# Kernel optimization log

Measured on AMD Instinct MI355X. Metric: run time of the kernel, lower is better.

## Reference

```python
import jax, jax.numpy as jnp
import numpy as np

WD, WH, WW = 4, 8, 8
N_WIN = WD * WH * WW  # 256 tokens per window
NUM_HEADS = 8
DIM = 512
HIDDEN = int(DIM * 4.0)
SHIFT = (2, 4, 4)
EPS = 1e-5


def _rel_pos_index():
    coords = np.stack(np.meshgrid(np.arange(WD), np.arange(WH), np.arange(WW), indexing='ij'))
    cf = coords.reshape(3, -1)  # [3, N]
    rc = cf[:, :, None] - cf[:, None, :]  # [3, N, N]
    rc = rc.transpose(1, 2, 0).astype(np.int64)
    rc[:, :, 0] += WD - 1
    rc[:, :, 1] += WH - 1
    rc[:, :, 2] += WW - 1
    rc[:, :, 0] *= (2 * WH - 1) * (2 * WW - 1)
    rc[:, :, 1] *= (2 * WW - 1)
    return jnp.asarray(rc.sum(-1))  # [N, N]

REL_IDX = _rel_pos_index()


def setup_inputs() -> dict:
    key = jax.random.key(0)
    ks = jax.random.split(key, 10)
    B, D, H, W = 1, 16, 64, 64
    L = D * H * W
    s = 0.02
    table_size = (2 * WD - 1) * (2 * WH - 1) * (2 * WW - 1)  # 1575
    return {
        'x': jax.random.normal(ks[0], (B, L, DIM), jnp.float32),
        't_emb': jax.random.normal(ks[1], (B, DIM), jnp.float32),
        'ada_w': jax.random.normal(ks[2], (DIM, 6 * DIM), jnp.float32) * s,
        'ada_b': jnp.zeros((6 * DIM,), jnp.float32),
        'rel_table': jax.random.normal(ks[3], (table_size, NUM_HEADS), jnp.float32) * s,
        'qkv_w': jax.random.normal(ks[4], (DIM, 3 * DIM), jnp.float32) * s,
        'qkv_b': jnp.zeros((3 * DIM,), jnp.float32),
        'proj_w': jax.random.normal(ks[5], (DIM, DIM), jnp.float32) * s,
        'proj_b': jnp.zeros((DIM,), jnp.float32),
        'fc1_w': jax.random.normal(ks[6], (DIM, HIDDEN), jnp.float32) * s,
        'fc1_b': jnp.zeros((HIDDEN,), jnp.float32),
        'fc2_w': jax.random.normal(ks[7], (HIDDEN, DIM), jnp.float32) * s,
        'fc2_b': jnp.zeros((DIM,), jnp.float32),
        'D': D, 'H': H, 'W': W,
    }


def _layernorm(y):
    m = jnp.mean(y, axis=-1, keepdims=True)
    v = jnp.mean(jnp.square(y - m), axis=-1, keepdims=True)
    return (y - m) * jax.lax.rsqrt(v + EPS)


def _window_partition(x3, D, H, W):
    B, _, _, _, C = x3.shape
    x3 = x3.reshape(B, D // WD, WD, H // WH, WH, W // WW, WW, C)
    x3 = x3.transpose(0, 1, 3, 5, 2, 4, 6, 7)
    return x3.reshape(-1, N_WIN, C)


def _window_reverse(win, B, D, H, W):
    C = win.shape[-1]
    x3 = win.reshape(B, D // WD, H // WH, W // WW, WD, WH, WW, C)
    x3 = x3.transpose(0, 1, 4, 2, 5, 3, 6, 7)
    return x3.reshape(B, D, H, W, C)


def _window_attention(xn, rel_table, qkv_w, qkv_b, proj_w, proj_b):
    Bn, N, C = xn.shape
    h, d = NUM_HEADS, C // NUM_HEADS
    qkv = (xn @ qkv_w + qkv_b).reshape(Bn, N, 3, h, d).transpose(2, 0, 3, 1, 4)
    q, k, v = qkv[0], qkv[1], qkv[2]
    scale = d ** -0.5
    attn = jnp.einsum('bhnd,bhmd->bhnm', q * scale, k)  # [Bn, h, N, N]
    bias = rel_table[REL_IDX]  # gather -> [N, N, h]
    attn = jax.nn.softmax(attn + bias.transpose(2, 0, 1)[None], axis=-1)
    o = jnp.einsum('bhnm,bhmd->bhnd', attn, v)
    o = o.transpose(0, 2, 1, 3).reshape(Bn, N, C)
    return o @ proj_w + proj_b


def reference(x, t_emb, ada_w, ada_b, rel_table, qkv_w, qkv_b, proj_w, proj_b,
              fc1_w, fc1_b, fc2_w, fc2_b, D, H, W):
    B, L, C = x.shape
    mod = jax.nn.silu(t_emb) @ ada_w + ada_b  # [B, 6C]
    shift_msa, scale_msa, gate_msa, shift_mlp, scale_mlp, gate_mlp = jnp.split(mod, 6, axis=-1)

    x3 = x.reshape(B, D, H, W, C)
    x3 = jnp.roll(x3, shift=(-SHIFT[0], -SHIFT[1], -SHIFT[2]), axis=(1, 2, 3))
    xw = _window_partition(x3, D, H, W)  # [B*nW, N, C]

    xn = _layernorm(xw) * (1.0 + scale_msa[:, None, :]) + shift_msa[:, None, :]
    attn_out = _window_attention(xn, rel_table, qkv_w, qkv_b, proj_w, proj_b)
    xw = xw + gate_msa[:, None, :] * attn_out

    x3 = _window_reverse(xw, B, D, H, W)
    x3 = jnp.roll(x3, shift=SHIFT, axis=(1, 2, 3))
    x = x3.reshape(B, L, C)

    xn = _layernorm(x) * (1.0 + scale_mlp[:, None, :]) + shift_mlp[:, None, :]
    h1 = jax.nn.gelu(xn @ fc1_w + fc1_b, approximate=False)
    mlp_out = h1 @ fc2_w + fc2_b
    return x + gate_mlp[:, None, :] * mlp_out
```

## Files before the change

### kernel.cpp

```cpp
#include <hip/hip_runtime.h>
#include <hip/hip_bf16.h>
#include <math.h>


typedef __attribute__((ext_vector_type(8))) short short8;
typedef __attribute__((ext_vector_type(4))) short bs4;
typedef __attribute__((ext_vector_type(4))) float f32x4;

typedef const __attribute__((address_space(1))) unsigned int gu32;
typedef __attribute__((address_space(3))) unsigned int lu32;

__device__ __forceinline__ float bf2f(short s) {
  unsigned int u = ((unsigned int)(unsigned short)s) << 16;
  float f;
  __builtin_memcpy(&f, &u, 4);
  return f;
}
__device__ __forceinline__ short f2bf(float f) {
  unsigned int u;
  __builtin_memcpy(&u, &f, 4);
  u += 0x7FFFu + ((u >> 16) & 1u);
  return (short)(u >> 16);
}
__device__ __forceinline__ short f2bf_trunc(float f) {
  unsigned int u;
  __builtin_memcpy(&u, &f, 4);
  return (short)(u >> 16);
}

__device__ __forceinline__ int win_to_src(int p) {
  int wi = p >> 8, t = p & 255;
  int sd = (((wi >> 6) << 2) + (t >> 6) + 2) & 15;
  int sh = ((((wi >> 3) & 7) << 3) + ((t >> 3) & 7) + 4) & 63;
  int sw = (((wi & 7) << 3) + (t & 7) + 4) & 63;
  return (sd << 12) | (sh << 6) | sw;
}

__global__ __launch_bounds__(256) void mod_kernel(
    const float* __restrict__ t_emb, const float* __restrict__ ada_w,
    const float* __restrict__ ada_b, float* __restrict__ mod) {
  __shared__ float sl[512];
  int tid = threadIdx.x;
  for (int r = 0; r < 2; ++r) {
    float x = t_emb[r * 256 + tid];
    sl[r * 256 + tid] = x / (1.f + expf(-x));
  }
  __syncthreads();
  int col = blockIdx.x * 256 + tid;
  float acc = ada_b[col];
  for (int k = 0; k < 512; ++k)
    acc += sl[k] * ada_w[(size_t)k * 3072 + col];
  mod[col] = acc;
}

__global__ __launch_bounds__(256) void bias_kernel(
    const float* __restrict__ rel_table, short* __restrict__ biasT) {
  int head = blockIdx.x >> 8;
  int j = blockIdx.x & 255;
  int i = threadIdx.x;
  int di = i >> 6, hi = (i >> 3) & 7, wi = i & 7;
  int dj = j >> 6, hj = (j >> 3) & 7, wj = j & 7;
  int idx = (di - dj + 3) * 225 + (hi - hj + 7) * 15 + (wi - wj + 7);
  biasT[(size_t)blockIdx.x * 256 + i] = f2bf(rel_table[idx * 8 + head]);
}

__global__ __launch_bounds__(256) void transpose_kernel(
    const float* __restrict__ in, short* __restrict__ out, int K, int N) {
  __shared__ short t[32][33];
  int n0 = blockIdx.x * 32, k0 = blockIdx.y * 32;
  int tx = threadIdx.x & 31, ty = threadIdx.x >> 5;
#pragma unroll
  for (int r = 0; r < 4; ++r)
    t[ty + r * 8][tx] = f2bf(in[(size_t)(k0 + ty + r * 8) * N + n0 + tx]);
  __syncthreads();
#pragma unroll
  for (int r = 0; r < 4; ++r)
    out[(size_t)(n0 + ty + r * 8) * K + k0 + tx] = t[tx][ty + r * 8];
}

template <int GATHER>
__global__ __launch_bounds__(256) void ln_kernel(
    const float* __restrict__ xin, short* __restrict__ xout,
    const float* __restrict__ shv, const float* __restrict__ scv) {
  int wave = threadIdx.x >> 6, lane = threadIdx.x & 63;
  int p = blockIdx.x * 4 + wave;
  int s = GATHER ? win_to_src(p) : p;
  const f32x4* px = (const f32x4*)(xin + (size_t)s * 512 + lane * 8);
  f32x4 a = px[0], b = px[1];
  float xs[8];
#pragma unroll
  for (int j = 0; j < 4; ++j) { xs[j] = a[j]; xs[4 + j] = b[j]; }
  float sum = 0.f, sq = 0.f;
#pragma unroll
  for (int j = 0; j < 8; ++j) { sum += xs[j]; sq += xs[j] * xs[j]; }
#pragma unroll
  for (int off = 1; off < 64; off <<= 1) {
    sum += __shfl_xor(sum, off, 64);
    sq += __shfl_xor(sq, off, 64);
  }
  float mean = sum * (1.f / 512.f);
  float var = sq * (1.f / 512.f) - mean * mean;
  float rs = rsqrtf(var + 1e-5f);
  short8 o;
#pragma unroll
  for (int j = 0; j < 8; ++j) {
    int c = lane * 8 + j;
    float val = (xs[j] - mean) * rs * (1.f + scv[c]) + shv[c];
    o[j] = f2bf(val);
  }
  *(short8*)(xout + (size_t)p * 512 + lane * 8) = o;
}

template <int EPI>
__global__ __launch_bounds__(256) void gemm_kernel(
    const short* __restrict__ A, const short* __restrict__ BT,
    const float* __restrict__ bias, void* __restrict__ Cv,
    int M, int N, int K, int nbn,
    const float* __restrict__ resid, const float* __restrict__ gate) {
  __shared__ __align__(16) short Atl[128 * 64];
  __shared__ __align__(16) short Btl[128 * 64];

  int nwg = gridDim.x;
  int bid = blockIdx.x;
  int q = nwg >> 3, r = nwg & 7;
  int xcd = bid & 7, idx = bid >> 3;
  int swz = (xcd < r ? xcd * (q + 1) : r * (q + 1) + (xcd - r) * q) + idx;
  int bm = swz / nbn, bn = swz % nbn;

  int tid = threadIdx.x;
  int lane = tid & 63, wave = tid >> 6;
  int l15 = lane & 15, lg = lane >> 4;
  int wr = (wave >> 1) * 64, wc = (wave & 1) * 64;

  const size_t rowb = (size_t)K * 2;
  const char* ga[4];
  const char* gb[4];
  char* la[4];
  char* lb[4];
#pragma unroll
  for (int rr = 0; rr < 4; ++rr) {
    int o = rr * 4096 + tid * 16;
    int so = o ^ (((o >> 7) & 7) << 4);
    int row = so >> 7, cb = so & 127;
    la[rr] = (char*)Atl + o;
    lb[rr] = (char*)Btl + o;
    ga[rr] = (const char*)A + (size_t)(bm * 128 + row) * rowb + cb;
    gb[rr] = (const char*)BT + (size_t)(bn * 128 + row) * rowb + cb;
  }

  f32x4 acc[4][4];
#pragma unroll
  for (int m = 0; m < 4; ++m)
#pragma unroll
    for (int n = 0; n < 4; ++n) acc[m][n] = (f32x4){0.f, 0.f, 0.f, 0.f};

  for (int kt = 0; kt < K; kt += 64) {
#pragma unroll
    for (int rr = 0; rr < 4; ++rr) {
      __builtin_amdgcn_global_load_lds((gu32*)ga[rr], (lu32*)la[rr], 16, 0, 0);
      __builtin_amdgcn_global_load_lds((gu32*)gb[rr], (lu32*)lb[rr], 16, 0, 0);
      ga[rr] += 128;
      gb[rr] += 128;
    }
    __syncthreads();

    short8 af[2][4], bfr[2][4];
    int swr = (l15 & 7) << 4;
#pragma unroll
    for (int m = 0; m < 4; ++m) {
      int base = (wr + m * 16 + l15) * 128;
#pragma unroll
      for (int ks = 0; ks < 2; ++ks)
        af[ks][m] = *(const short8*)((const char*)Atl + base + ((ks * 64 + lg * 16) ^ swr));
    }
#pragma unroll
    for (int n = 0; n < 4; ++n) {
      int base = (wc + n * 16 + l15) * 128;
#pragma unroll
      for (int ks = 0; ks < 2; ++ks)
        bfr[ks][n] = *(const short8*)((const char*)Btl + base + ((ks * 64 + lg * 16) ^ swr));
    }
#pragma unroll
    for (int ks = 0; ks < 2; ++ks)
#pragma unroll
      for (int m = 0; m < 4; ++m)
#pragma unroll
        for (int n = 0; n < 4; ++n)
          acc[m][n] = __builtin_amdgcn_mfma_f32_16x16x32_bf16(af[ks][m], bfr[ks][n], acc[m][n], 0, 0, 0);
    __syncthreads();
  }

#pragma unroll
  for (int m = 0; m < 4; ++m)
#pragma unroll
    for (int n = 0; n < 4; ++n) {
      int col = bn * 128 + wc + n * 16 + l15;
      float bv = bias[col];
#pragma unroll
      for (int i = 0; i < 4; ++i) {
        int row = bm * 128 + wr + m * 16 + lg * 4 + i;
        float v = acc[m][n][i] + bv;
        if (EPI == 0) {
          ((short*)Cv)[(size_t)row * N + col] = f2bf(v);
        } else if (EPI == 1) {
          v = 0.5f * v * (1.f + erff(v * 0.70710678118f));
          ((short*)Cv)[(size_t)row * N + col] = f2bf(v);
        } else if (EPI == 2) {
          int s = win_to_src(row);
          float xv = resid[(size_t)s * 512 + col];
          ((float*)Cv)[(size_t)s * 512 + col] = xv + gate[col] * v;
        } else {
          float xv = resid[(size_t)row * 512 + col];
          ((float*)Cv)[(size_t)row * 512 + col] = xv + gate[col] * v;
        }
      }
    }
}

__global__ __launch_bounds__(256) void attn_kernel(
    const short* __restrict__ qkv, const short* __restrict__ biasT,
    short* __restrict__ aout) {
  __shared__ __align__(16) short vt[64][264];
  __shared__ __align__(16) short pl[4][64][40];
  int win = blockIdx.x, head = blockIdx.y;
  int tid = threadIdx.x, lane = tid & 63, wave = tid >> 6;
  int l15 = lane & 15, lg = lane >> 4;
  const short* qp = qkv + (size_t)win * 256 * 1536 + head * 64;
  const short* kp = qp + 512;
  const short* vp = qp + 1024;

#pragma unroll
  for (int r = 0; r < 8; ++r) {
    short8 vv = *(const short8*)(vp + (size_t)tid * 1536 + r * 8);
#pragma unroll
    for (int j = 0; j < 8; ++j) vt[r * 8 + j][tid] = vv[j];
  }

  short8 qf[4][2];
#pragma unroll
  for (int m = 0; m < 4; ++m)
#pragma unroll
    for (int kk = 0; kk < 2; ++kk)
      qf[m][kk] = *(const short8*)(qp + (size_t)(wave * 64 + m * 16 + l15) * 1536 + kk * 32 + lg * 8);

  __syncthreads();

  float mrun[4][4], lrun[4][4];
  f32x4 ao[4][4];
#pragma unroll
  for (int m = 0; m < 4; ++m)
#pragma unroll
    for (int i = 0; i < 4; ++i) { mrun[m][i] = -1e30f; lrun[m][i] = 0.f; }
#pragma unroll
  for (int m = 0; m < 4; ++m)
#pragma unroll
    for (int n = 0; n < 4; ++n) ao[m][n] = (f32x4){0.f, 0.f, 0.f, 0.f};

  for (int kc = 0; kc < 4; ++kc) {
    f32x4 sv[4][4];
#pragma unroll
    for (int m = 0; m < 4; ++m)
#pragma unroll
      for (int n = 0; n < 4; ++n) sv[m][n] = (f32x4){0.f, 0.f, 0.f, 0.f};
#pragma unroll
    for (int n = 0; n < 4; ++n)
#pragma unroll
      for (int kk = 0; kk < 2; ++kk) {
        short8 kf = *(const short8*)(kp + (size_t)(kc * 64 + n * 16 + l15) * 1536 + kk * 32 + lg * 8);
#pragma unroll
        for (int m = 0; m < 4; ++m)
          sv[m][n] = __builtin_amdgcn_mfma_f32_16x16x32_bf16(qf[m][kk], kf, sv[m][n], 0, 0, 0);
      }
#pragma unroll
    for (int n = 0; n < 4; ++n) {
      const short* bq = biasT + (size_t)(head * 256 + kc * 64 + n * 16 + l15) * 256 + wave * 64 + lg * 4;
#pragma unroll
      for (int m = 0; m < 4; ++m) {
        bs4 bt = *(const bs4*)(bq + m * 16);
#pragma unroll
        for (int i = 0; i < 4; ++i)
          sv[m][n][i] = sv[m][n][i] * 0.125f + bf2f(bt[i]);
      }
    }
#pragma unroll
    for (int m = 0; m < 4; ++m)
#pragma unroll
      for (int i = 0; i < 4; ++i) {
        float mx = fmaxf(fmaxf(sv[m][0][i], sv[m][1][i]), fmaxf(sv[m][2][i], sv[m][3][i]));
#pragma unroll
        for (int off = 1; off < 16; off <<= 1) mx = fmaxf(mx, __shfl_xor(mx, off, 64));
        float nm = fmaxf(mrun[m][i], mx);
        float corr = __expf(mrun[m][i] - nm);
        mrun[m][i] = nm;
        float rs = 0.f;
#pragma unroll
        for (int n = 0; n < 4; ++n) {
          float pe = __expf(sv[m][n][i] - nm);
          sv[m][n][i] = pe;
          rs += pe;
        }
#pragma unroll
        for (int off = 1; off < 16; off <<= 1) rs += __shfl_xor(rs, off, 64);
        lrun[m][i] = lrun[m][i] * corr + rs;
#pragma unroll
        for (int n = 0; n < 4; ++n) ao[m][n][i] *= corr;
      }
#pragma unroll
    for (int s = 0; s < 2; ++s) {
#pragma unroll
      for (int m = 0; m < 4; ++m)
#pragma unroll
        for (int nn = 0; nn < 2; ++nn) {
          int n = 2 * s + nn;
#pragma unroll
          for (int i = 0; i < 4; ++i)
            pl[wave][m * 16 + lg * 4 + i][nn * 16 + l15] = f2bf_trunc(sv[m][n][i]);
        }
      short8 pf[4];
#pragma unroll
      for (int m = 0; m < 4; ++m)
        pf[m] = *(const short8*)&pl[wave][m * 16 + l15][lg * 8];
#pragma unroll
      for (int n2 = 0; n2 < 4; ++n2) {
        short8 vf = *(const short8*)&vt[n2 * 16 + l15][kc * 64 + s * 32 + lg * 8];
#pragma unroll
        for (int m = 0; m < 4; ++m)
          ao[m][n2] = __builtin_amdgcn_mfma_f32_16x16x32_bf16(pf[m], vf, ao[m][n2], 0, 0, 0);
      }
    }
  }

#pragma unroll
  for (int m = 0; m < 4; ++m)
#pragma unroll
    for (int i = 0; i < 4; ++i) {
      float inv = 1.f / lrun[m][i];
      int row = win * 256 + wave * 64 + m * 16 + lg * 4 + i;
#pragma unroll
      for (int n = 0; n < 4; ++n)
        aout[(size_t)row * 512 + head * 64 + n * 16 + l15] = f2bf(ao[m][n][i] * inv);
    }
}

extern "C" void kernel_launch(void* const* d_in, const int* in_sizes, int n_in,
                              void* d_out, int out_size, void* d_ws, size_t ws_size,
                              hipStream_t stream) {
  (void)in_sizes; (void)n_in; (void)out_size; (void)ws_size;
  const float* x         = (const float*)d_in[0];
  const float* t_emb     = (const float*)d_in[1];
  const float* ada_w     = (const float*)d_in[2];
  const float* ada_b     = (const float*)d_in[3];
  const float* rel_table = (const float*)d_in[4];
  const float* qkv_w     = (const float*)d_in[5];
  const float* qkv_b     = (const float*)d_in[6];
  const float* proj_w    = (const float*)d_in[7];
  const float* proj_b    = (const float*)d_in[8];
  const float* fc1_w     = (const float*)d_in[9];
  const float* fc1_b     = (const float*)d_in[10];
  const float* fc2_w     = (const float*)d_in[11];
  const float* fc2_b     = (const float*)d_in[12];
  float* out = (float*)d_out;
  char* ws = (char*)d_ws;

  float* mod    = (float*)(ws);
  short* biasT  = (short*)(ws + 16384);
  short* qkvwT  = (short*)(ws + 16384 + 2097152);
  short* projwT = qkvwT + 1536 * 512;
  short* fc1wT  = projwT + 512 * 512;
  short* fc2wT  = fc1wT + 2048 * 512;
  short* xn     = (short*)(ws + 8404992);
  short* qkvb   = xn + (size_t)65536 * 512;
  short* attno  = qkvb + (size_t)65536 * 1536;
  short* h1     = qkvb;
  float* x2     = out;

  mod_kernel<<<12, 256, 0, stream>>>(t_emb, ada_w, ada_b, mod);
  bias_kernel<<<2048, 256, 0, stream>>>(rel_table, biasT);
  transpose_kernel<<<dim3(48, 16), 256, 0, stream>>>(qkv_w, qkvwT, 512, 1536);
  transpose_kernel<<<dim3(16, 16), 256, 0, stream>>>(proj_w, projwT, 512, 512);
  transpose_kernel<<<dim3(64, 16), 256, 0, stream>>>(fc1_w, fc1wT, 512, 2048);
  transpose_kernel<<<dim3(16, 64), 256, 0, stream>>>(fc2_w, fc2wT, 2048, 512);

  ln_kernel<1><<<16384, 256, 0, stream>>>(x, xn, mod + 0, mod + 512);
  gemm_kernel<0><<<512 * 12, 256, 0, stream>>>(xn, qkvwT, qkv_b, qkvb,
                                               65536, 1536, 512, 12, nullptr, nullptr);
  attn_kernel<<<dim3(256, 8), 256, 0, stream>>>(qkvb, biasT, attno);
  gemm_kernel<2><<<512 * 4, 256, 0, stream>>>(attno, projwT, proj_b, x2,
                                              65536, 512, 512, 4, x, mod + 1024);
  ln_kernel<0><<<16384, 256, 0, stream>>>(x2, xn, mod + 1536, mod + 2048);
  gemm_kernel<1><<<512 * 16, 256, 0, stream>>>(xn, fc1wT, fc1_b, h1,
                                               65536, 2048, 512, 16, nullptr, nullptr);
  gemm_kernel<3><<<512 * 4, 256, 0, stream>>>(h1, fc2wT, fc2_b, out,
                                              65536, 512, 2048, 4, x2, mod + 2560);
}
```

Before: 1.040 ms.

## Double-buffer GEMM LDS tiles and use tanh-form GELU in the fc1 epilogue

```diff
diff --git a/kernel.cpp b/kernel.cpp
--- a/kernel.cpp
+++ b/kernel.cpp
@@ -117,8 +117,8 @@
     const float* __restrict__ bias, void* __restrict__ Cv,
     int M, int N, int K, int nbn,
     const float* __restrict__ resid, const float* __restrict__ gate) {
-  __shared__ __align__(16) short Atl[128 * 64];
-  __shared__ __align__(16) short Btl[128 * 64];
+  __shared__ __align__(16) short Atl[2][128 * 64];
+  __shared__ __align__(16) short Btl[2][128 * 64];
 
   int nwg = gridDim.x;
   int bid = blockIdx.x;
@@ -135,15 +135,13 @@
   const size_t rowb = (size_t)K * 2;
   const char* ga[4];
   const char* gb[4];
-  char* la[4];
-  char* lb[4];
+  int lo[4];
 #pragma unroll
   for (int rr = 0; rr < 4; ++rr) {
     int o = rr * 4096 + tid * 16;
     int so = o ^ (((o >> 7) & 7) << 4);
     int row = so >> 7, cb = so & 127;
-    la[rr] = (char*)Atl + o;
-    lb[rr] = (char*)Btl + o;
+    lo[rr] = o;
     ga[rr] = (const char*)A + (size_t)(bm * 128 + row) * rowb + cb;
     gb[rr] = (const char*)BT + (size_t)(bn * 128 + row) * rowb + cb;
   }
@@ -154,31 +152,32 @@
 #pragma unroll
     for (int n = 0; n < 4; ++n) acc[m][n] = (f32x4){0.f, 0.f, 0.f, 0.f};
 
-  for (int kt = 0; kt < K; kt += 64) {
+  const int swr = (l15 & 7) << 4;
+
+  auto stage = [&](int buf) {
 #pragma unroll
     for (int rr = 0; rr < 4; ++rr) {
-      __builtin_amdgcn_global_load_lds((gu32*)ga[rr], (lu32*)la[rr], 16, 0, 0);
-      __builtin_amdgcn_global_load_lds((gu32*)gb[rr], (lu32*)lb[rr], 16, 0, 0);
+      __builtin_amdgcn_global_load_lds((gu32*)ga[rr], (lu32*)((char*)Atl[buf] + lo[rr]), 16, 0, 0);
+      __builtin_amdgcn_global_load_lds((gu32*)gb[rr], (lu32*)((char*)Btl[buf] + lo[rr]), 16, 0, 0);
       ga[rr] += 128;
       gb[rr] += 128;
     }
-    __syncthreads();
-
+  };
+  auto compute = [&](int buf) {
     short8 af[2][4], bfr[2][4];
-    int swr = (l15 & 7) << 4;
 #pragma unroll
     for (int m = 0; m < 4; ++m) {
       int base = (wr + m * 16 + l15) * 128;
 #pragma unroll
       for (int ks = 0; ks < 2; ++ks)
-        af[ks][m] = *(const short8*)((const char*)Atl + base + ((ks * 64 + lg * 16) ^ swr));
+        af[ks][m] = *(const short8*)((const char*)Atl[buf] + base + ((ks * 64 + lg * 16) ^ swr));
     }
 #pragma unroll
     for (int n = 0; n < 4; ++n) {
       int base = (wc + n * 16 + l15) * 128;
 #pragma unroll
       for (int ks = 0; ks < 2; ++ks)
-        bfr[ks][n] = *(const short8*)((const char*)Btl + base + ((ks * 64 + lg * 16) ^ swr));
+        bfr[ks][n] = *(const short8*)((const char*)Btl[buf] + base + ((ks * 64 + lg * 16) ^ swr));
     }
 #pragma unroll
     for (int ks = 0; ks < 2; ++ks)
@@ -187,8 +186,19 @@
 #pragma unroll
         for (int n = 0; n < 4; ++n)
           acc[m][n] = __builtin_amdgcn_mfma_f32_16x16x32_bf16(af[ks][m], bfr[ks][n], acc[m][n], 0, 0, 0);
+  };
+
+  const int nt = K >> 6;
+  stage(0);
+  __syncthreads();
+  int cur = 0;
+  for (int t = 0; t + 1 < nt; ++t) {
+    stage(cur ^ 1);
+    compute(cur);
     __syncthreads();
-  }
+    cur ^= 1;
+  }
+  compute(cur);
 
 #pragma unroll
   for (int m = 0; m < 4; ++m)
@@ -203,8 +213,9 @@
         if (EPI == 0) {
           ((short*)Cv)[(size_t)row * N + col] = f2bf(v);
         } else if (EPI == 1) {
-          v = 0.5f * v * (1.f + erff(v * 0.70710678118f));
-          ((short*)Cv)[(size_t)row * N + col] = f2bf(v);
+          float tt = v * (0.7978845608f + 0.0356774081f * v * v);
+          float sg = 1.f / (1.f + __expf(-2.f * tt));
+          ((short*)Cv)[(size_t)row * N + col] = f2bf_trunc(v * sg);
         } else if (EPI == 2) {
           int s = win_to_src(row);
           float xv = resid[(size_t)s * 512 + col];
```

Result: slower. 1.073 ms (+3.2%).
